# Performance work log

Measured on AMD Instinct MI355X. Metric: run time of the kernel, lower is better.

The kernel has to match this reference:

```python
import jax, jax.numpy as jnp
import numpy as np


def conv2d(x, w, b, pad=1):
    y = jax.lax.conv_general_dilated(x, w, (1, 1), [(pad, pad), (pad, pad)],
                                     dimension_numbers=('NCHW', 'OIHW', 'NCHW'))
    return y + b[None, :, None, None]


def deform_conv2d(x, offsets, w, b, groups=8, pad=1):
    # torchvision-style deformable conv: offsets [B, 2*G*K, H, W] laid out as
    # (g, k, (dy, dx)); input channels split into G offset groups; zero padding
    # outside the image for bilinear sampling.
    B, C, H, W = x.shape
    kh, kw = w.shape[2], w.shape[3]
    K = kh * kw
    cpg = C // groups
    off = offsets.reshape(B, groups, K, 2, H, W)
    dy, dx = off[:, :, :, 0], off[:, :, :, 1]  # [B,G,K,H,W]
    ky, kx = jnp.meshgrid(jnp.arange(kh), jnp.arange(kw), indexing='ij')
    ky = ky.reshape(K).astype(x.dtype)
    kx = kx.reshape(K).astype(x.dtype)
    ygrid = jnp.arange(H, dtype=x.dtype)
    xgrid = jnp.arange(W, dtype=x.dtype)
    # absolute sampling positions [B,G,K,H,W]
    py = ygrid[None, None, None, :, None] + (ky - pad)[None, None, :, None, None] + dy
    px = xgrid[None, None, None, None, :] + (kx - pad)[None, None, :, None, None] + dx
    y0 = jnp.floor(py)
    x0 = jnp.floor(px)
    wy = py - y0  # frac weights [B,G,K,H,W]
    wx = px - x0
    y0i = y0.astype(jnp.int32)
    x0i = x0.astype(jnp.int32)
    xg = x.reshape(B, groups, cpg, H * W)

    def gather(yc, xc):
        valid = ((yc >= 0) & (yc < H) & (xc >= 0) & (xc < W)).astype(x.dtype)
        idx = jnp.clip(yc, 0, H - 1) * W + jnp.clip(xc, 0, W - 1)
        idx = jnp.broadcast_to(idx.reshape(B, groups, 1, K * H * W),
                               (B, groups, cpg, K * H * W))
        v = jnp.take_along_axis(xg, idx, axis=3).reshape(B, groups, cpg, K, H, W)
        return v * valid[:, :, None]

    v00 = gather(y0i, x0i)
    v01 = gather(y0i, x0i + 1)
    v10 = gather(y0i + 1, x0i)
    v11 = gather(y0i + 1, x0i + 1)
    wy_ = wy[:, :, None]  # [B,G,1,K,H,W]
    wx_ = wx[:, :, None]
    sampled = (v00 * (1 - wy_) * (1 - wx_) + v01 * (1 - wy_) * wx_
               + v10 * wy_ * (1 - wx_) + v11 * wy_ * wx_)
    sampled = sampled.reshape(B, C, K, H, W)
    out = jnp.einsum('bckhw,ock->bohw', sampled, w.reshape(w.shape[0], C, K))
    return out + b[None, :, None, None]


def dab(feat, aux_in, aux_w, aux_b, fw1, fb1, fw2, fb2, se_w1, se_b1, se_w2, se_b2):
    # Adaptive fusion block: project aux (128->64), concat, conv-relu-conv body,
    # SE channel attention (reduction=2), residual add onto feat.
    aux = jax.nn.relu(conv2d(aux_in, aux_w, aux_b))
    x = jnp.concatenate([feat, aux], axis=1)  # [B,128,H,W]
    x = jax.nn.relu(conv2d(x, fw1, fb1))      # 128->64
    x = conv2d(x, fw2, fb2)                   # 64->64
    g = jnp.mean(x, axis=(2, 3))              # [B,64]
    a = jax.nn.sigmoid(jax.nn.relu(g @ se_w1.T + se_b1) @ se_w2.T + se_b2)
    return feat + x * a[:, :, None, None]


def setup_inputs() -> dict:
    key = jax.random.key(0)
    ks = jax.random.split(key, 16)
    B, H, W = 4, 192, 192

    def p(k, shape, s=0.05):
        return jax.random.normal(k, shape, jnp.float32) * s

    return {
        'mv': jax.random.normal(ks[0], (B, 128, H, W), jnp.float32),
        'ref_feature': jax.random.normal(ks[1], (B, 64, H, W), jnp.float32),
        'head_w': p(ks[2], (144, 128, 3, 3)), 'head_b': jnp.zeros((144,), jnp.float32),
        'dcn_w': p(ks[3], (64, 64, 3, 3)), 'dcn_b': jnp.zeros((64,), jnp.float32),
        'c1w1': p(ks[4], (128, 64, 3, 3)), 'c1b1': jnp.zeros((128,), jnp.float32),
        'c1w2': p(ks[5], (128, 128, 3, 3)), 'c1b2': jnp.zeros((128,), jnp.float32),
        'aux_w': p(ks[6], (64, 128, 3, 3)), 'aux_b': jnp.zeros((64,), jnp.float32),
        'fw1': p(ks[7], (64, 128, 3, 3)), 'fb1': jnp.zeros((64,), jnp.float32),
        'fw2': p(ks[8], (64, 64, 3, 3)), 'fb2': jnp.zeros((64,), jnp.float32),
        'se_w1': p(ks[9], (32, 64)), 'se_b1': jnp.zeros((32,), jnp.float32),
        'se_w2': p(ks[10], (64, 32)), 'se_b2': jnp.zeros((64,), jnp.float32),
    }


def reference(mv, ref_feature, head_w, head_b, dcn_w, dcn_b, c1w1, c1b1, c1w2, c1b2,
              aux_w, aux_b, fw1, fb1, fw2, fb2, se_w1, se_b1, se_w2, se_b2):
    offsets = conv2d(mv, head_w, head_b)                       # [B,144,H,W]
    def_feat = jax.nn.relu(deform_conv2d(ref_feature, offsets, dcn_w, dcn_b))
    aux_in = jax.nn.relu(conv2d(jax.nn.relu(conv2d(ref_feature, c1w1, c1b1)),
                                c1w2, c1b2))                   # convs1: 64->128->128
    return dab(def_feat, aux_in, aux_w, aux_b, fw1, fb1, fw2, fb2,
               se_w1, se_b1, se_w2, se_b2)
```

## Files before the change

kernel.cpp:

```cpp
#include <hip/hip_runtime.h>
#include <math.h>

#define HH 192
#define WW 192
#define HWSZ (HH*WW)
#define BB 4

typedef __attribute__((ext_vector_type(8))) short bf16x8;
typedef __attribute__((ext_vector_type(4))) float f32x4;

__device__ __forceinline__ unsigned short f2bf(float f) {
    unsigned int u = __float_as_uint(f);
    u = (u + 0x7FFFu + ((u >> 16) & 1u)) >> 16;
    return (unsigned short)u;
}
__device__ __forceinline__ float bf2f(unsigned short s) {
    return __uint_as_float(((unsigned int)s) << 16);
}

__global__ void prep_all(
    const float* __restrict__ head_w, const float* __restrict__ c1w1,
    const float* __restrict__ c1w2,   const float* __restrict__ aux_w,
    const float* __restrict__ fw1,    const float* __restrict__ fw2,
    const float* __restrict__ dcn_w,
    unsigned short* __restrict__ wb_head, unsigned short* __restrict__ wb_c1w1,
    unsigned short* __restrict__ wb_c1w2, unsigned short* __restrict__ wb_aux,
    unsigned short* __restrict__ wb_fw1,  unsigned short* __restrict__ wb_fw2,
    unsigned short* __restrict__ wdefb2)
{
    int idx = blockIdx.x * 256 + threadIdx.x;
    const float* w; unsigned short* wb; int cout, cin;
    if (idx < 165888)                 { w = head_w; wb = wb_head; cout = 144; cin = 128; }
    else if ((idx -= 165888) < 73728) { w = c1w1;   wb = wb_c1w1; cout = 128; cin = 64;  }
    else if ((idx -= 73728) < 147456) { w = c1w2;   wb = wb_c1w2; cout = 128; cin = 128; }
    else if ((idx -= 147456) < 73728) { w = aux_w;  wb = wb_aux;  cout = 64;  cin = 128; }
    else if ((idx -= 73728) < 73728)  { w = fw1;    wb = wb_fw1;  cout = 64;  cin = 128; }
    else if ((idx -= 73728) < 36864)  { w = fw2;    wb = wb_fw2;  cout = 64;  cin = 64;  }
    else if ((idx -= 36864) < 36864) {
        int o = idx / 576, rem = idx % 576;
        int c = rem / 9, k = rem - c * 9;
        int K = k * 64 + c;
        wdefb2[((size_t)((K >> 5) * 64 + o)) * 32 + (K & 31)] = f2bf(dcn_w[idx]);
        return;
    } else return;
    int o = idx / (cin * 9);
    int rem = idx - o * cin * 9;
    int c = rem / 9;
    int t = rem - c * 9;
    int nch = cin >> 5;
    wb[((t * nch + (c >> 5)) * cout + o) * 32 + (c & 31)] = f2bf(w[idx]);
}

__global__ __launch_bounds__(256) void transpose_all(
    const float* __restrict__ mv, const float* __restrict__ ref,
    unsigned short* __restrict__ mvb, unsigned short* __restrict__ refb)
{
    __shared__ float tile[32][68];
    const int tid = threadIdx.x;
    int bz = blockIdx.z;
    const float* in; unsigned short* outb;
    if (bz < 16) { in = mv;  outb = mvb;  }
    else         { in = ref; outb = refb; bz -= 16; }
    const int y = blockIdx.y;
    const int x0 = blockIdx.x * 64;
#pragma unroll
    for (int it = 0; it < 2; ++it) {
        int u = tid + it * 256;
        int c = u >> 4, q = u & 15;
        float4 v = *(const float4*)(in + (((size_t)bz * 32 + c) * HH + y) * WW + x0 + q * 4);
        *(float4*)&tile[c][q * 4] = v;
    }
    __syncthreads();
    const int pxl = tid >> 2, c8 = tid & 3;
    bf16x8 ov;
#pragma unroll
    for (int j = 0; j < 8; ++j) ov[j] = (short)f2bf(tile[c8 * 8 + j][pxl]);
    *(bf16x8*)(outb + (((size_t)bz * HH + y) * WW + x0 + pxl) * 32 + c8 * 8) = ov;
}

template<int CIN, int COUT_TILE, bool RELU, int EPI>
__global__ __launch_bounds__(256, 3) void conv3x3_v10(
    const unsigned short* __restrict__ in, const unsigned short* __restrict__ wb,
    const float* __restrict__ bias, void* __restrict__ outp,
    int cTot, int ocBase, int nOc, int coutFull, int nPerXcd)
{
    constexpr int NCH = CIN / 32;
    constexpr int NOC = COUT_TILE / 16;
    constexpr int WGR = 36 * COUT_TILE;
    __shared__ __align__(16) unsigned short sx[6 * 72 * 32];
    __shared__ __align__(16) unsigned short sw[288 * COUT_TILE];

    const int tid = threadIdx.x;
    const int d = blockIdx.x;
    const int w = (d & 7) * nPerXcd + (d >> 3);
    const int ocT = (w % nOc) * COUT_TILE;
    int t = w / nOc;
    const int x0 = (t % 3) * 64; t /= 3;
    const int y0 = (t % 48) * 4;
    const int b  = t / 48;
    const int wv = tid >> 6, lane = tid & 63;
    const int l15 = lane & 15, kg = lane >> 4;

    f32x4 acc[NOC][4];
#pragma unroll
    for (int oc = 0; oc < NOC; ++oc)
#pragma unroll
        for (int s = 0; s < 4; ++s) acc[oc][s] = (f32x4){0.f, 0.f, 0.f, 0.f};

    for (int ch = 0; ch < NCH; ++ch) {
#pragma unroll
        for (int it = 0; it < 7; ++it) {
            int u = tid + it * 256;
            if (u < 1728) {
                int r = u / 288;
                int rem = u - r * 288;
                int px = rem >> 2, c8 = rem & 3;
                int yin = y0 - 1 + r;
                int gx  = x0 - 4 + px;
                bf16x8 v = {0,0,0,0,0,0,0,0};
                if (yin >= 0 && yin < HH && gx >= 0 && gx < WW)
                    v = *(const bf16x8*)(in + (((size_t)(b * NCH + ch) * HH + yin) * WW + gx) * 32 + c8 * 8);
                *(bf16x8*)&sx[(r * 72 + px) * 32 + ((c8 ^ ((px >> 1) & 3)) << 3)] = v;
            }
        }
#pragma unroll
        for (int it = 0; it < 7; ++it) {
            int u = tid + it * 256;
            if (u < WGR) {
                int tap = u / (4 * COUT_TILE);
                int rem = u - tap * 4 * COUT_TILE;
                int kgi = rem / COUT_TILE;
                int row = rem - kgi * COUT_TILE;
                bf16x8 v = *(const bf16x8*)(wb
                    + ((size_t)((tap * NCH + ch) * coutFull) + ocT + row) * 32 + kgi * 8);
                *(bf16x8*)&sw[((tap * 4 + kgi) * COUT_TILE + row) * 8] = v;
            }
        }
        __syncthreads();
#pragma unroll
        for (int ky = 0; ky < 3; ++ky) {
#pragma unroll
            for (int kx = 0; kx < 3; ++kx) {
                const int r = wv + ky;
                const int tap = ky * 3 + kx;
                bf16x8 bf[4];
#pragma unroll
                for (int s = 0; s < 4; ++s) {
                    int p = s * 16 + l15 + kx + 3;
                    bf[s] = *(const bf16x8*)&sx[(r * 72 + p) * 32 + ((kg ^ ((p >> 1) & 3)) << 3)];
                }
#pragma unroll
                for (int oc = 0; oc < NOC; ++oc) {
                    bf16x8 a = *(const bf16x8*)&sw[((tap * 4 + kg) * COUT_TILE + oc * 16 + l15) * 8];
#pragma unroll
                    for (int s = 0; s < 4; ++s)
                        acc[oc][s] = __builtin_amdgcn_mfma_f32_16x16x32_bf16(a, bf[s], acc[oc][s], 0, 0, 0);
                }
            }
        }
        __syncthreads();
    }
    const int y = y0 + wv;
    if (EPI == 1) {
        float* out = (float*)outp;
#pragma unroll
        for (int oc = 0; oc < NOC; ++oc)
#pragma unroll
            for (int s = 0; s < 4; ++s) {
                int xo = x0 + s * 16 + l15;
#pragma unroll
                for (int j = 0; j < 4; ++j) {
                    int oL = ocT + oc * 16 + kg * 4 + j;
                    float rv = acc[oc][s][j] + bias[oL];
                    if (RELU) rv = fmaxf(rv, 0.f);
                    out[((size_t)(b * cTot + ocBase + oL) * HH + y) * WW + xo] = rv;
                }
            }
    } else if (EPI == 2) {
        unsigned short* out = (unsigned short*)outp;
#pragma unroll
        for (int oc = 0; oc < NOC; ++oc)
#pragma unroll
            for (int s = 0; s < 4; ++s) {
                int xo = x0 + s * 16 + l15;
#pragma unroll
                for (int j = 0; j < 4; ++j) {
                    int oL = ocT + oc * 16 + kg * 4 + j;
                    float rv = acc[oc][s][j] + bias[oL];
                    if (RELU) rv = fmaxf(rv, 0.f);
                    out[((size_t)(b * cTot + ocBase + oL) * HH + y) * WW + xo] = f2bf(rv);
                }
            }
    } else {
        unsigned short* out = (unsigned short*)outp;
#pragma unroll
        for (int oc = 0; oc < NOC; ++oc) {
            int oL = ocT + oc * 16 + kg * 4;
            int o0 = ocBase + oL;
#pragma unroll
            for (int s = 0; s < 4; ++s) {
                int xo = x0 + s * 16 + l15;
                ushort4 u;
                float r0 = acc[oc][s][0] + bias[oL + 0];
                float r1 = acc[oc][s][1] + bias[oL + 1];
                float r2 = acc[oc][s][2] + bias[oL + 2];
                float r3 = acc[oc][s][3] + bias[oL + 3];
                if (RELU) { r0 = fmaxf(r0,0.f); r1 = fmaxf(r1,0.f); r2 = fmaxf(r2,0.f); r3 = fmaxf(r3,0.f); }
                u.x = f2bf(r0); u.y = f2bf(r1); u.z = f2bf(r2); u.w = f2bf(r3);
                *(ushort4*)(out + ((((size_t)(b * cTot + (o0 >> 5)) * HH + y) * WW + xo) * 32) + (o0 & 31)) = u;
            }
        }
    }
}

__global__ __launch_bounds__(512, 4) void deform_v6(
    const unsigned short* __restrict__ xb, const unsigned short* __restrict__ offb,
    const unsigned short* __restrict__ wdefb2, const float* __restrict__ bias,
    unsigned short* __restrict__ cat)
{
    __shared__ __align__(16) unsigned short smp[64 * 584];
    const int tid = threadIdx.x;
    const int b = blockIdx.z;
    int flat = blockIdx.x;
    int nf = (flat & 7) * 72 + (flat >> 3);
    const int pixbase = nf * 64;

    const int px = tid & 63, g = tid >> 6;
    const int pix = pixbase + px;
    const int y = pix / WW, x = pix - y * WW;

    const char* xgb = (const char*)(xb + ((size_t)(b * 2 + (g >> 2)) * HWSZ) * 32 + (g & 3) * 8);
    const unsigned short* ob = offb + ((size_t)(b * 144 + g * 18)) * HWSZ + pix;

    float dyv[9], dxv[9];
#pragma unroll
    for (int k = 0; k < 9; ++k) {
        dyv[k] = bf2f(ob[(size_t)(2 * k) * HWSZ]);
        dxv[k] = bf2f(ob[(size_t)(2 * k + 1) * HWSZ]);
    }

    auto calc = [&](int k, int vo[4], float w4[4]) {
        float pyf = (float)(y + k / 3 - 1) + dyv[k];
        float pxf = (float)(x + k % 3 - 1) + dxv[k];
        float fy = floorf(pyf), fx = floorf(pxf);
        float wy = pyf - fy, wx = pxf - fx;
        int iy = (int)fy, ix = (int)fx;
        float w00 = (1.f - wy) * (1.f - wx), w01 = (1.f - wy) * wx;
        float w10 = wy * (1.f - wx),         w11 = wy * wx;
        bool y0v = (iy >= 0) && (iy < HH);
        bool y1v = (iy + 1 >= 0) && (iy + 1 < HH);
        bool x0v = (ix >= 0) && (ix < WW);
        bool x1v = (ix + 1 >= 0) && (ix + 1 < WW);
        if (!(y0v && x0v)) w00 = 0.f;
        if (!(y0v && x1v)) w01 = 0.f;
        if (!(y1v && x0v)) w10 = 0.f;
        if (!(y1v && x1v)) w11 = 0.f;
        int cy0 = min(max(iy, 0), HH - 1), cy1 = min(max(iy + 1, 0), HH - 1);
        int cx0 = min(max(ix, 0), WW - 1), cx1 = min(max(ix + 1, 0), WW - 1);
        vo[0] = (cy0 * WW + cx0) * 64;
        vo[1] = (cy0 * WW + cx1) * 64;
        vo[2] = (cy1 * WW + cx0) * 64;
        vo[3] = (cy1 * WW + cx1) * 64;
        w4[0] = w00; w4[1] = w01; w4[2] = w10; w4[3] = w11;
    };

    float wr[3][4];
    bf16x8 pf[2][4];
    {
        int vo[4]; calc(0, vo, wr[0]);
#pragma unroll
        for (int j = 0; j < 4; ++j) pf[0][j] = *(const bf16x8*)(xgb + vo[j]);
    }
    {
        int vo[4]; calc(1, vo, wr[1]);
#pragma unroll
        for (int j = 0; j < 4; ++j) pf[1][j] = *(const bf16x8*)(xgb + vo[j]);
    }
    unsigned short* so = smp + px * 584 + g * 8;
#pragma unroll
    for (int k = 0; k < 9; ++k) {
        bf16x8 nx0, nx1, nx2, nx3;
        if (k + 2 < 9) {
            int vo[4]; calc(k + 2, vo, wr[(k + 2) % 3]);
            nx0 = *(const bf16x8*)(xgb + vo[0]);
            nx1 = *(const bf16x8*)(xgb + vo[1]);
            nx2 = *(const bf16x8*)(xgb + vo[2]);
            nx3 = *(const bf16x8*)(xgb + vo[3]);
        }
        __builtin_amdgcn_sched_barrier(0);
        bf16x8 ov;
#pragma unroll
        for (int cc = 0; cc < 8; ++cc) {
            float s = bf2f((unsigned short)pf[k & 1][0][cc]) * wr[k % 3][0]
                    + bf2f((unsigned short)pf[k & 1][1][cc]) * wr[k % 3][1]
                    + bf2f((unsigned short)pf[k & 1][2][cc]) * wr[k % 3][2]
                    + bf2f((unsigned short)pf[k & 1][3][cc]) * wr[k % 3][3];
            ov[cc] = (short)f2bf(s);
        }
        *(bf16x8*)(so + k * 64) = ov;
        if (k + 2 < 9) { pf[k & 1][0] = nx0; pf[k & 1][1] = nx1; pf[k & 1][2] = nx2; pf[k & 1][3] = nx3; }
    }
    __syncthreads();
    const int wv = tid >> 6;
    const int lane = tid & 63, l15 = lane & 15, kg = lane >> 4;
    const int oc = wv >> 1, sp = (wv & 1) * 2;
    f32x4 acc0 = (f32x4){0.f, 0.f, 0.f, 0.f};
    f32x4 acc1 = (f32x4){0.f, 0.f, 0.f, 0.f};
    const unsigned short* arow = wdefb2 + ((size_t)(oc * 16 + l15)) * 32 + kg * 8;
#pragma unroll
    for (int ch = 0; ch < 18; ++ch) {
        bf16x8 b0 = *(const bf16x8*)&smp[(sp * 16 + l15) * 584 + ch * 32 + kg * 8];
        bf16x8 b1 = *(const bf16x8*)&smp[((sp + 1) * 16 + l15) * 584 + ch * 32 + kg * 8];
        bf16x8 a = *(const bf16x8*)(arow + (size_t)ch * 64 * 32);
        acc0 = __builtin_amdgcn_mfma_f32_16x16x32_bf16(a, b0, acc0, 0, 0, 0);
        acc1 = __builtin_amdgcn_mfma_f32_16x16x32_bf16(a, b1, acc1, 0, 0, 0);
    }
    const int o0 = oc * 16 + kg * 4;
#pragma unroll
    for (int s = 0; s < 2; ++s) {
        const f32x4& av = s ? acc1 : acc0;
        int pxo = pixbase + (sp + s) * 16 + l15;
        int yo = pxo / WW, xo = pxo - yo * WW;
        ushort4 u;
        u.x = f2bf(fmaxf(av[0] + bias[o0 + 0], 0.f));
        u.y = f2bf(fmaxf(av[1] + bias[o0 + 1], 0.f));
        u.z = f2bf(fmaxf(av[2] + bias[o0 + 2], 0.f));
        u.w = f2bf(fmaxf(av[3] + bias[o0 + 3], 0.f));
        *(ushort4*)(cat + ((((size_t)(b * 4 + (o0 >> 5)) * HH + yo) * WW + xo) * 32) + (o0 & 31)) = u;
    }
}

__global__ __launch_bounds__(256) void pool_kernel(const float* __restrict__ x, float* __restrict__ gout)
{
    int bc = blockIdx.x;
    const float* p = x + (size_t)bc * HWSZ;
    int tid = threadIdx.x;
    float s = 0.f;
    for (int i = tid * 4; i < HWSZ; i += 256 * 4) {
        float4 v = *reinterpret_cast<const float4*>(p + i);
        s += v.x + v.y + v.z + v.w;
    }
#pragma unroll
    for (int o = 32; o > 0; o >>= 1) s += __shfl_down(s, o, 64);
    __shared__ float red[4];
    if ((tid & 63) == 0) red[tid >> 6] = s;
    __syncthreads();
    if (tid == 0) gout[bc] = (red[0] + red[1] + red[2] + red[3]) * (1.f / (float)HWSZ);
}

__global__ __launch_bounds__(256) void se_kernel(
    const float* __restrict__ g, const float* __restrict__ w1, const float* __restrict__ b1,
    const float* __restrict__ w2, const float* __restrict__ b2, float* __restrict__ a)
{
    __shared__ float sg[BB * 64];
    __shared__ float sh[BB * 32];
    int tid = threadIdx.x;
    sg[tid] = g[tid];
    __syncthreads();
    if (tid < BB * 32) {
        int b = tid / 32, h = tid % 32;
        float s = b1[h];
        for (int c = 0; c < 64; ++c) s += sg[b * 64 + c] * w1[h * 64 + c];
        sh[b * 32 + h] = fmaxf(s, 0.f);
    }
    __syncthreads();
    {
        int b = tid / 64, o = tid % 64;
        float s = b2[o];
        for (int h = 0; h < 32; ++h) s += sh[b * 32 + h] * w2[o * 32 + h];
        a[tid] = 1.f / (1.f + expf(-s));
    }
}

__global__ __launch_bounds__(256) void final_v2(
    float* __restrict__ out, const unsigned short* __restrict__ catb, const float* __restrict__ a)
{
    const int VPC = HWSZ / 4;
    int v = blockIdx.x * 256 + threadIdx.x;
    int bc = v / VPC, within = v - bc * VPC;
    int b = bc >> 6, c = bc & 63;
    float av = a[bc];
    int pix = within * 4;
    int y = pix / WW, x = pix - y * WW;
    const unsigned short* dbase = catb
        + (((size_t)(b * 4 + (c >> 5)) * HH + y) * WW + x) * 32 + (c & 31);
    float4 xo = reinterpret_cast<float4*>(out)[v];
    float4 r;
    r.x = bf2f(dbase[0])  + xo.x * av;
    r.y = bf2f(dbase[32]) + xo.y * av;
    r.z = bf2f(dbase[64]) + xo.z * av;
    r.w = bf2f(dbase[96]) + xo.w * av;
    reinterpret_cast<float4*>(out)[v] = r;
}

extern "C" void kernel_launch(void* const* d_in, const int* in_sizes, int n_in,
                              void* d_out, int out_size, void* d_ws, size_t ws_size,
                              hipStream_t stream) {
    const float* mv     = (const float*)d_in[0];
    const float* ref    = (const float*)d_in[1];
    const float* head_w = (const float*)d_in[2];
    const float* head_b = (const float*)d_in[3];
    const float* dcn_w  = (const float*)d_in[4];
    const float* dcn_b  = (const float*)d_in[5];
    const float* c1w1   = (const float*)d_in[6];
    const float* c1b1   = (const float*)d_in[7];
    const float* c1w2   = (const float*)d_in[8];
    const float* c1b2   = (const float*)d_in[9];
    const float* aux_w  = (const float*)d_in[10];
    const float* aux_b  = (const float*)d_in[11];
    const float* fw1    = (const float*)d_in[12];
    const float* fb1    = (const float*)d_in[13];
    const float* fw2    = (const float*)d_in[14];
    const float* fb2    = (const float*)d_in[15];
    const float* se_w1  = (const float*)d_in[16];
    const float* se_b1  = (const float*)d_in[17];
    const float* se_w2  = (const float*)d_in[18];
    const float* se_b2  = (const float*)d_in[19];
    float* out = (float*)d_out;

    float* ws = (float*)d_ws;
    unsigned short* offb     = (unsigned short*)ws;
    unsigned short* mvb      = (unsigned short*)(ws + 21233664);
    unsigned short* refb     = (unsigned short*)(ws + 30670848);
    unsigned short* catb     = (unsigned short*)(ws + 35389440);
    unsigned short* r2b      = (unsigned short*)(ws + 44826624);
    unsigned short* wdefb2   = (unsigned short*)(ws + 54263808);
    unsigned short* wbb      = (unsigned short*)(ws + 54282240);
    float* gbuf              = ws + 54567936;
    float* abuf              = gbuf + 256;
    unsigned short* t1b      = (unsigned short*)ws;

    unsigned short* wb_head = wbb;
    unsigned short* wb_c1w1 = wb_head + 165888;
    unsigned short* wb_c1w2 = wb_c1w1 + 73728;
    unsigned short* wb_aux  = wb_c1w2 + 147456;
    unsigned short* wb_fw1  = wb_aux  + 73728;
    unsigned short* wb_fw2  = wb_fw1  + 73728;

    prep_all<<<2376, 256, 0, stream>>>(head_w, c1w1, c1w2, aux_w, fw1, fw2, dcn_w,
                                       wb_head, wb_c1w1, wb_c1w2, wb_aux, wb_fw1, wb_fw2, wdefb2);
    transpose_all<<<dim3(3, 192, 24), 256, 0, stream>>>(mv, ref, mvb, refb);

    conv3x3_v10<128, 48, false, 2><<<1728, 256, 0, stream>>>(
        mvb, wb_head, head_b, offb, 144, 0, 3, 144, 216);
    deform_v6<<<dim3(576, 1, BB), 512, 0, stream>>>(refb, offb, wdefb2, dcn_b, catb);
    conv3x3_v10<64, 32, true, 0><<<2304, 256, 0, stream>>>(
        refb, wb_c1w1, c1b1, t1b, 4, 0, 4, 128, 288);
    conv3x3_v10<128, 32, true, 0><<<2304, 256, 0, stream>>>(
        t1b, wb_c1w2, c1b2, r2b, 4, 0, 4, 128, 288);
    conv3x3_v10<128, 32, true, 0><<<1152, 256, 0, stream>>>(
        r2b, wb_aux, aux_b, catb, 4, 64, 2, 64, 144);
    conv3x3_v10<128, 32, true, 0><<<1152, 256, 0, stream>>>(
        catb, wb_fw1, fb1, r2b, 2, 0, 2, 64, 144);
    conv3x3_v10<64, 32, false, 1><<<1152, 256, 0, stream>>>(
        r2b, wb_fw2, fb2, out, 64, 0, 2, 64, 144);
    pool_kernel<<<BB * 64, 256, 0, stream>>>(out, gbuf);
    se_kernel<<<1, 256, 0, stream>>>(gbuf, se_w1, se_b1, se_w2, se_b2, abuf);
    final_v2<<<9216, 256, 0, stream>>>(out, catb, abuf);
}
```

Measured before the change: 449.8 us.

## Merge prep kernels, fuse global pooling into last conv, widen conv output tiles

Folds the weight-conversion and input-transpose kernels into a single launch that also zeroes the pooling buffer. The separate pool kernel is removed: the final conv epilogue accumulates per-channel partial sums and adds them with atomics, and the SE kernel applies the mean scaling. Conv output-channel tiles grow from 32 to 64, which halves the number of blocks and reuses each input tile across more outputs. Occupancy hint drops to 2 per SIMD. The cost is more register and LDS pressure plus atomic contention on the pooled sums.

Result: slower. 499.0 us (+10.9%).

```diff
diff --git a/kernel.cpp b/kernel.cpp
--- a/kernel.cpp
+++ b/kernel.cpp
@@ -18,7 +18,9 @@
     return __uint_as_float(((unsigned int)s) << 16);
 }
 
-__global__ void prep_all(
+__global__ __launch_bounds__(256) void prep_merged(
+    const float* __restrict__ mv, const float* __restrict__ ref,
+    unsigned short* __restrict__ mvb, unsigned short* __restrict__ refb,
     const float* __restrict__ head_w, const float* __restrict__ c1w1,
     const float* __restrict__ c1w2,   const float* __restrict__ aux_w,
     const float* __restrict__ fw1,    const float* __restrict__ fw2,
@@ -26,9 +28,36 @@
     unsigned short* __restrict__ wb_head, unsigned short* __restrict__ wb_c1w1,
     unsigned short* __restrict__ wb_c1w2, unsigned short* __restrict__ wb_aux,
     unsigned short* __restrict__ wb_fw1,  unsigned short* __restrict__ wb_fw2,
-    unsigned short* __restrict__ wdefb2)
+    unsigned short* __restrict__ wdefb2,  float* __restrict__ gbuf)
 {
-    int idx = blockIdx.x * 256 + threadIdx.x;
+    __shared__ float tile[32][68];
+    const int tid = threadIdx.x;
+    int bid = blockIdx.x;
+    if (bid < 13824) {
+        int bz = bid / 576;
+        int rem = bid - bz * 576;
+        const int y = rem / 3;
+        const int x0 = (rem % 3) * 64;
+        const float* in; unsigned short* outb;
+        if (bz < 16) { in = mv;  outb = mvb;  }
+        else         { in = ref; outb = refb; bz -= 16; }
+#pragma unroll
+        for (int it = 0; it < 2; ++it) {
+            int u = tid + it * 256;
+            int c = u >> 4, q = u & 15;
+            float4 v = *(const float4*)(in + (((size_t)bz * 32 + c) * HH + y) * WW + x0 + q * 4);
+            *(float4*)&tile[c][q * 4] = v;
+        }
+        __syncthreads();
+        const int pxl = tid >> 2, c8 = tid & 3;
+        bf16x8 ov;
+#pragma unroll
+        for (int j = 0; j < 8; ++j) ov[j] = (short)f2bf(tile[c8 * 8 + j][pxl]);
+        *(bf16x8*)(outb + (((size_t)bz * HH + y) * WW + x0 + pxl) * 32 + c8 * 8) = ov;
+        return;
+    }
+    if (bid == 16200) { gbuf[tid] = 0.f; return; }
+    int idx = (bid - 13824) * 256 + tid;
     const float* w; unsigned short* wb; int cout, cin;
     if (idx < 165888)                 { w = head_w; wb = wb_head; cout = 144; cin = 128; }
     else if ((idx -= 165888) < 73728) { w = c1w1;   wb = wb_c1w1; cout = 128; cin = 64;  }
@@ -51,42 +80,17 @@
     wb[((t * nch + (c >> 5)) * cout + o) * 32 + (c & 31)] = f2bf(w[idx]);
 }
 
-__global__ __launch_bounds__(256) void transpose_all(
-    const float* __restrict__ mv, const float* __restrict__ ref,
-    unsigned short* __restrict__ mvb, unsigned short* __restrict__ refb)
-{
-    __shared__ float tile[32][68];
-    const int tid = threadIdx.x;
-    int bz = blockIdx.z;
-    const float* in; unsigned short* outb;
-    if (bz < 16) { in = mv;  outb = mvb;  }
-    else         { in = ref; outb = refb; bz -= 16; }
-    const int y = blockIdx.y;
-    const int x0 = blockIdx.x * 64;
-#pragma unroll
-    for (int it = 0; it < 2; ++it) {
-        int u = tid + it * 256;
-        int c = u >> 4, q = u & 15;
-        float4 v = *(const float4*)(in + (((size_t)bz * 32 + c) * HH + y) * WW + x0 + q * 4);
-        *(float4*)&tile[c][q * 4] = v;
-    }
-    __syncthreads();
-    const int pxl = tid >> 2, c8 = tid & 3;
-    bf16x8 ov;
-#pragma unroll
-    for (int j = 0; j < 8; ++j) ov[j] = (short)f2bf(tile[c8 * 8 + j][pxl]);
-    *(bf16x8*)(outb + (((size_t)bz * HH + y) * WW + x0 + pxl) * 32 + c8 * 8) = ov;
-}
-
-template<int CIN, int COUT_TILE, bool RELU, int EPI>
-__global__ __launch_bounds__(256, 3) void conv3x3_v10(
+template<int CIN, int COUT_TILE, bool RELU, int EPI, bool POOL>
+__global__ __launch_bounds__(256, 2) void conv3x3_v11(
     const unsigned short* __restrict__ in, const unsigned short* __restrict__ wb,
     const float* __restrict__ bias, void* __restrict__ outp,
-    int cTot, int ocBase, int nOc, int coutFull, int nPerXcd)
+    int cTot, int ocBase, int nOc, int coutFull, int nPerXcd,
+    float* __restrict__ gbuf)
 {
     constexpr int NCH = CIN / 32;
     constexpr int NOC = COUT_TILE / 16;
     constexpr int WGR = 36 * COUT_TILE;
+    constexpr int WIT = (WGR + 255) / 256;
     __shared__ __align__(16) unsigned short sx[6 * 72 * 32];
     __shared__ __align__(16) unsigned short sw[288 * COUT_TILE];
 
@@ -124,7 +128,7 @@
             }
         }
 #pragma unroll
-        for (int it = 0; it < 7; ++it) {
+        for (int it = 0; it < WIT; ++it) {
             int u = tid + it * 256;
             if (u < WGR) {
                 int tap = u / (4 * COUT_TILE);
@@ -163,6 +167,11 @@
     const int y = y0 + wv;
     if (EPI == 1) {
         float* out = (float*)outp;
+        float ps[NOC][4];
+#pragma unroll
+        for (int oc = 0; oc < NOC; ++oc)
+#pragma unroll
+            for (int j = 0; j < 4; ++j) ps[oc][j] = 0.f;
 #pragma unroll
         for (int oc = 0; oc < NOC; ++oc)
 #pragma unroll
@@ -174,8 +183,21 @@
                     float rv = acc[oc][s][j] + bias[oL];
                     if (RELU) rv = fmaxf(rv, 0.f);
                     out[((size_t)(b * cTot + ocBase + oL) * HH + y) * WW + xo] = rv;
+                    if (POOL) ps[oc][j] += rv;
                 }
             }
+        if (POOL) {
+#pragma unroll
+            for (int oc = 0; oc < NOC; ++oc)
+#pragma unroll
+                for (int j = 0; j < 4; ++j) {
+                    float v = ps[oc][j];
+#pragma unroll
+                    for (int m = 1; m < 16; m <<= 1) v += __shfl_xor(v, m, 64);
+                    if (l15 == 0)
+                        atomicAdd(&gbuf[b * 64 + ocT + oc * 16 + kg * 4 + j], v);
+                }
+        }
     } else if (EPI == 2) {
         unsigned short* out = (unsigned short*)outp;
 #pragma unroll
@@ -330,24 +352,6 @@
     }
 }
 
-__global__ __launch_bounds__(256) void pool_kernel(const float* __restrict__ x, float* __restrict__ gout)
-{
-    int bc = blockIdx.x;
-    const float* p = x + (size_t)bc * HWSZ;
-    int tid = threadIdx.x;
-    float s = 0.f;
-    for (int i = tid * 4; i < HWSZ; i += 256 * 4) {
-        float4 v = *reinterpret_cast<const float4*>(p + i);
-        s += v.x + v.y + v.z + v.w;
-    }
-#pragma unroll
-    for (int o = 32; o > 0; o >>= 1) s += __shfl_down(s, o, 64);
-    __shared__ float red[4];
-    if ((tid & 63) == 0) red[tid >> 6] = s;
-    __syncthreads();
-    if (tid == 0) gout[bc] = (red[0] + red[1] + red[2] + red[3]) * (1.f / (float)HWSZ);
-}
-
 __global__ __launch_bounds__(256) void se_kernel(
     const float* __restrict__ g, const float* __restrict__ w1, const float* __restrict__ b1,
     const float* __restrict__ w2, const float* __restrict__ b2, float* __restrict__ a)
@@ -355,7 +359,7 @@
     __shared__ float sg[BB * 64];
     __shared__ float sh[BB * 32];
     int tid = threadIdx.x;
-    sg[tid] = g[tid];
+    sg[tid] = g[tid] * (1.f / (float)HWSZ);
     __syncthreads();
     if (tid < BB * 32) {
         int b = tid / 32, h = tid % 32;
@@ -437,24 +441,23 @@
     unsigned short* wb_fw1  = wb_aux  + 73728;
     unsigned short* wb_fw2  = wb_fw1  + 73728;
 
-    prep_all<<<2376, 256, 0, stream>>>(head_w, c1w1, c1w2, aux_w, fw1, fw2, dcn_w,
-                                       wb_head, wb_c1w1, wb_c1w2, wb_aux, wb_fw1, wb_fw2, wdefb2);
-    transpose_all<<<dim3(3, 192, 24), 256, 0, stream>>>(mv, ref, mvb, refb);
-
-    conv3x3_v10<128, 48, false, 2><<<1728, 256, 0, stream>>>(
-        mvb, wb_head, head_b, offb, 144, 0, 3, 144, 216);
+    prep_merged<<<16201, 256, 0, stream>>>(mv, ref, mvb, refb,
+        head_w, c1w1, c1w2, aux_w, fw1, fw2, dcn_w,
+        wb_head, wb_c1w1, wb_c1w2, wb_aux, wb_fw1, wb_fw2, wdefb2, gbuf);
+
+    conv3x3_v11<128, 48, false, 2, false><<<1728, 256, 0, stream>>>(
+        mvb, wb_head, head_b, offb, 144, 0, 3, 144, 216, nullptr);
     deform_v6<<<dim3(576, 1, BB), 512, 0, stream>>>(refb, offb, wdefb2, dcn_b, catb);
-    conv3x3_v10<64, 32, true, 0><<<2304, 256, 0, stream>>>(
-        refb, wb_c1w1, c1b1, t1b, 4, 0, 4, 128, 288);
-    conv3x3_v10<128, 32, true, 0><<<2304, 256, 0, stream>>>(
-        t1b, wb_c1w2, c1b2, r2b, 4, 0, 4, 128, 288);
-    conv3x3_v10<128, 32, true, 0><<<1152, 256, 0, stream>>>(
-        r2b, wb_aux, aux_b, catb, 4, 64, 2, 64, 144);
-    conv3x3_v10<128, 32, true, 0><<<1152, 256, 0, stream>>>(
-        catb, wb_fw1, fb1, r2b, 2, 0, 2, 64, 144);
-    conv3x3_v10<64, 32, false, 1><<<1152, 256, 0, stream>>>(
-        r2b, wb_fw2, fb2, out, 64, 0, 2, 64, 144);
-    pool_kernel<<<BB * 64, 256, 0, stream>>>(out, gbuf);
+    conv3x3_v11<64, 64, true, 0, false><<<1152, 256, 0, stream>>>(
+        refb, wb_c1w1, c1b1, t1b, 4, 0, 2, 128, 144, nullptr);
+    conv3x3_v11<128, 64, true, 0, false><<<1152, 256, 0, stream>>>(
+        t1b, wb_c1w2, c1b2, r2b, 4, 0, 2, 128, 144, nullptr);
+    conv3x3_v11<128, 64, true, 0, false><<<576, 256, 0, stream>>>(
+        r2b, wb_aux, aux_b, catb, 4, 64, 1, 64, 72, nullptr);
+    conv3x3_v11<128, 64, true, 0, false><<<576, 256, 0, stream>>>(
+        catb, wb_fw1, fb1, r2b, 2, 0, 1, 64, 72, nullptr);
+    conv3x3_v11<64, 64, false, 1, true><<<576, 256, 0, stream>>>(
+        r2b, wb_fw2, fb2, out, 64, 0, 1, 64, 72, gbuf);
     se_kernel<<<1, 256, 0, stream>>>(gbuf, se_w1, se_b1, se_w2, se_b2, abuf);
     final_v2<<<9216, 256, 0, stream>>>(out, catb, abuf);
 }
```
